# Kernel tuning notes

Measured on AMD Instinct MI355X. Metric: run time of the kernel, lower is better.

The kernel has to match this reference:

```python
import jax, jax.numpy as jnp
import numpy as np

N_NODES = 100000
N_EDGES = 1600000
IN_DIM = 128
HIDDEN = 128
N_CLASSES = 10
N_GRAPHS = 64


def _inv_sqrt_deg(deg):
    # DGL norm='both': 1/sqrt(deg), with inf (deg==0) clamped to 0
    return jnp.where(deg > 0, jax.lax.rsqrt(jnp.maximum(deg, 1.0)), 0.0)


def graph_conv(h, src, dst, W, b):
    # DGL GraphConv, norm='both': rst = D_in^{-1/2} A D_out^{-1/2} h W + b
    ones = jnp.ones((src.shape[0],), dtype=h.dtype)
    deg_out = jax.ops.segment_sum(ones, src, num_segments=N_NODES)
    deg_in = jax.ops.segment_sum(ones, dst, num_segments=N_NODES)
    h = h * _inv_sqrt_deg(deg_out)[:, None]          # src-side norm
    msg = h[src]                                      # gather [E, D]
    agg = jax.ops.segment_sum(msg, dst, num_segments=N_NODES)  # scatter-add
    agg = agg * _inv_sqrt_deg(deg_in)[:, None]        # dst-side norm
    return agg @ W + b


def avg_pool(h, graph_ids):
    sums = jax.ops.segment_sum(h, graph_ids, num_segments=N_GRAPHS)
    cnt = jax.ops.segment_sum(jnp.ones((h.shape[0],), h.dtype), graph_ids,
                              num_segments=N_GRAPHS)
    return sums / jnp.maximum(cnt, 1.0)[:, None]


def setup_inputs() -> dict:
    key = jax.random.key(0)
    ks = jax.random.split(key, 10)
    h = jax.random.normal(ks[0], (N_NODES, IN_DIM), dtype=jnp.float32)
    src = jax.random.randint(ks[1], (N_EDGES,), 0, N_NODES)
    dst = jax.random.randint(ks[2], (N_EDGES,), 0, N_NODES)
    graph_ids = jnp.sort(jax.random.randint(ks[3], (N_NODES,), 0, N_GRAPHS))
    s1 = 1.0 / np.sqrt(IN_DIM)
    s2 = 1.0 / np.sqrt(HIDDEN)
    W1 = jax.random.uniform(ks[4], (IN_DIM, HIDDEN), jnp.float32, -s1, s1)
    b1 = jnp.zeros((HIDDEN,), jnp.float32)
    W2 = jax.random.uniform(ks[5], (HIDDEN, HIDDEN), jnp.float32, -s2, s2)
    b2 = jnp.zeros((HIDDEN,), jnp.float32)
    Wc = jax.random.uniform(ks[6], (HIDDEN, N_CLASSES), jnp.float32, -s2, s2)
    bc = jnp.zeros((N_CLASSES,), jnp.float32)
    return {"h": h, "src": src, "dst": dst, "graph_ids": graph_ids,
            "W1": W1, "b1": b1, "W2": W2, "b2": b2, "Wc": Wc, "bc": bc}


def reference(h, src, dst, graph_ids, W1, b1, W2, b2, Wc, bc):
    h = jax.nn.relu(graph_conv(h, src, dst, W1, b1))
    h = jax.nn.relu(graph_conv(h, src, dst, W2, b2))
    hg = avg_pool(h, graph_ids)          # [N_GRAPHS, HIDDEN]
    return hg @ Wc + bc                  # [N_GRAPHS, N_CLASSES]
```

## Files before the change

kernel.cpp:

```cpp
#include <hip/hip_runtime.h>

#define N_NODES 100000
#define N_EDGES 1600000
#define DIM     128
#define NGRAPH  64
#define NCLS    10
#define ZROW    N_NODES

#define NBLK    64
#define EPB     (N_EDGES / NBLK)
#define RANGE   50000

typedef __bf16 bf16x8 __attribute__((ext_vector_type(8)));
typedef float  f32x4  __attribute__((ext_vector_type(4)));

__device__ __forceinline__ ushort f2bf(float x) {
  uint b = __float_as_uint(x);
  b += 0x7fffu + ((b >> 16) & 1u);
  return (ushort)(b >> 16);
}
__device__ __forceinline__ uint pack2(float lo, float hi) {
  return (uint)f2bf(lo) | ((uint)f2bf(hi) << 16);
}
__device__ __forceinline__ float unlo(uint u) { return __uint_as_float(u << 16); }
__device__ __forceinline__ float unhi(uint u) { return __uint_as_float(u & 0xffff0000u); }

__device__ __forceinline__ void acc8(float* a, uint4 u) {
  a[0] += unlo(u.x); a[1] += unhi(u.x);
  a[2] += unlo(u.y); a[3] += unhi(u.y);
  a[4] += unlo(u.z); a[5] += unhi(u.z);
  a[6] += unlo(u.w); a[7] += unhi(u.w);
}

__global__ void k_init(float* __restrict__ pool, float* __restrict__ cnt,
                       uint* __restrict__ padrow) {
  int t = threadIdx.x;
  for (int i = t; i < NGRAPH * DIM; i += 256) pool[i] = 0.f;
  if (t < NGRAPH) cnt[t] = 0.f;
  if (t < DIM / 2) padrow[t] = 0u;
}

__global__ __launch_bounds__(256)
void k_hist(const int* __restrict__ src, const int* __restrict__ dst,
            ushort* __restrict__ part) {
  extern __shared__ uint cnt[];
  int p = blockIdx.y;
  int b = blockIdx.x;
  const int* ids = (p < 2) ? dst : src;
  int base = (p & 1) * RANGE;
  for (int i = threadIdx.x; i < RANGE / 2; i += 256) cnt[i] = 0;
  __syncthreads();
  int cb = b * EPB;
  for (int j = threadIdx.x; j < EPB; j += 256) {
    int v = ids[cb + j] - base;
    if ((unsigned)v < RANGE) atomicAdd(&cnt[v >> 1], 1u << ((v & 1) * 16));
  }
  __syncthreads();
  uint* out = (uint*)(part + ((size_t)p * NBLK + b) * RANGE);
  for (int i = threadIdx.x; i < RANGE / 2; i += 256) out[i] = cnt[i];
}

__global__ void k_degsum(const ushort* __restrict__ part, int* __restrict__ deg_in,
                         int* __restrict__ deg_out, ushort* __restrict__ pre) {
  int n = blockIdx.x * 256 + threadIdx.x;
  if (n >= N_NODES) return;
  int r = n / RANGE, i = n % RANGE;
  const ushort* pin  = part + ((size_t)r * NBLK) * RANGE + i;
  const ushort* pout = part + ((size_t)(2 + r) * NBLK) * RANGE + i;
  int sin = 0, sout = 0;
  for (int b = 0; b < NBLK; ++b) {
    pre[(size_t)b * N_NODES + n] = (ushort)sin;
    sin  += pin[(size_t)b * RANGE];
    sout += pout[(size_t)b * RANGE];
  }
  deg_in[n] = sin;
  deg_out[n] = sout;
}

__global__ void k_blocksum(const int* __restrict__ deg_in, int* __restrict__ bsum) {
  __shared__ int s[256];
  int i = blockIdx.x * 256 + threadIdx.x;
  s[threadIdx.x] = (i < N_NODES) ? deg_in[i] : 0;
  __syncthreads();
  for (int off = 128; off > 0; off >>= 1) {
    if (threadIdx.x < off) s[threadIdx.x] += s[threadIdx.x + off];
    __syncthreads();
  }
  if (threadIdx.x == 0) bsum[blockIdx.x] = s[0];
}

__global__ void k_scan_bsum(int* __restrict__ bsum, int nb) {
  __shared__ int s[512];
  int t = threadIdx.x;
  int v = (t < nb) ? bsum[t] : 0;
  s[t] = v;
  __syncthreads();
  for (int off = 1; off < 512; off <<= 1) {
    int x = (t >= off) ? s[t - off] : 0;
    __syncthreads();
    s[t] += x;
    __syncthreads();
  }
  if (t < nb) bsum[t] = s[t] - v;
}

__global__ void k_rowptr(const int* __restrict__ deg_in, const int* __restrict__ bsum,
                         int* __restrict__ row_ptr) {
  __shared__ int s[256];
  int t = threadIdx.x;
  int i = blockIdx.x * 256 + t;
  int v = (i < N_NODES) ? deg_in[i] : 0;
  s[t] = v;
  __syncthreads();
  for (int off = 1; off < 256; off <<= 1) {
    int x = (t >= off) ? s[t - off] : 0;
    __syncthreads();
    s[t] += x;
    __syncthreads();
  }
  if (i < N_NODES) row_ptr[i] = bsum[blockIdx.x] + s[t] - v;
  if (i == N_NODES - 1) row_ptr[N_NODES] = bsum[blockIdx.x] + s[t];
}

__global__ __launch_bounds__(256)
void k_fillrank(const int* __restrict__ src, const int* __restrict__ dst,
                const int* __restrict__ row_ptr, const ushort* __restrict__ pre,
                int* __restrict__ csr_src) {
  extern __shared__ uint rk[];
  int b = blockIdx.x;
  int base = blockIdx.y * RANGE;
  for (int i = threadIdx.x; i < RANGE / 2; i += 256) rk[i] = 0;
  __syncthreads();
  int cb = b * EPB;
  for (int j = threadIdx.x; j < EPB; j += 256) {
    int d = dst[cb + j];
    int s = src[cb + j];
    int v = d - base;
    if ((unsigned)v < RANGE) {
      uint old = atomicAdd(&rk[v >> 1], 1u << ((v & 1) * 16));
      int rank = (old >> ((v & 1) * 16)) & 0xffff;
      int pos = row_ptr[d] + pre[(size_t)b * N_NODES + d] + rank;
      csr_src[pos] = s;
    }
  }
}

__global__ void k_convW(const float* __restrict__ W1, const float* __restrict__ W2,
                        ushort* __restrict__ Wt1, ushort* __restrict__ Wt2) {
  int idx = blockIdx.x * 256 + threadIdx.x;
  const float* W = (idx < 16384) ? W1 : W2;
  ushort* Wt = (idx < 16384) ? Wt1 : Wt2;
  int t = idx & 16383;
  int c = t >> 7, k = t & 127;
  Wt[c * 128 + k] = f2bf(W[k * 128 + c]);
}

__global__ void k_prescale(const float4* __restrict__ h4, const int* __restrict__ deg_out,
                           uint4* __restrict__ out4) {
  int idx = blockIdx.x * blockDim.x + threadIdx.x;
  if (idx < N_NODES * 16) {
    int row = idx >> 4;
    int d = deg_out[row];
    float s = d > 0 ? rsqrtf((float)d) : 0.f;
    float4 v0 = h4[idx * 2];
    float4 v1 = h4[idx * 2 + 1];
    uint4 o;
    o.x = pack2(v0.x * s, v0.y * s);
    o.y = pack2(v0.z * s, v0.w * s);
    o.z = pack2(v1.x * s, v1.y * s);
    o.w = pack2(v1.z * s, v1.w * s);
    out4[idx] = o;
  }
}

__global__ __launch_bounds__(256)
void k_gg(const uint* __restrict__ hs, const int* __restrict__ row_ptr,
          const int* __restrict__ csr_src, const ushort* __restrict__ Wt,
          const float* __restrict__ bias, const int* __restrict__ deg_scale,
          ushort* __restrict__ out) {
  __shared__ ushort As[16][136];
  int wv = threadIdx.x >> 6, lane = threadIdx.x & 63;
  int strip = blockIdx.x;
  int sub = lane >> 4, li = lane & 15;

  int lr = lane & 15, lk = lane >> 4;
  bf16x8 bfrag[4][2];
  #pragma unroll
  for (int ks = 0; ks < 4; ++ks)
    #pragma unroll
    for (int c2 = 0; c2 < 2; ++c2)
      bfrag[ks][c2] = *(const bf16x8*)(Wt + (size_t)((wv * 2 + c2) * 16 + lr) * 128 +
                                       ks * 32 + lk * 8);

  #pragma unroll
  for (int it = 0; it < 4; ++it) {
    int n = strip * 16 + wv * 4 + it;
    int beg = row_ptr[n], end = row_ptr[n + 1], deg = end - beg;
    float a[8] = {};
    for (int cb2 = 0; cb2 < deg; cb2 += 64) {
      int cdeg = min(64, deg - cb2);
      int myidx = (lane < cdeg) ? csr_src[beg + cb2 + lane] : ZROW;
      for (int e = 0; e < cdeg; e += 16) {
        int s0 = __shfl(myidx, e + sub);
        int s1 = __shfl(myidx, e + 4 + sub);
        int s2 = __shfl(myidx, e + 8 + sub);
        int s3 = __shfl(myidx, e + 12 + sub);
        uint4 u0 = *(const uint4*)(hs + (size_t)s0 * 64 + li * 4);
        uint4 u1 = *(const uint4*)(hs + (size_t)s1 * 64 + li * 4);
        uint4 u2 = *(const uint4*)(hs + (size_t)s2 * 64 + li * 4);
        uint4 u3 = *(const uint4*)(hs + (size_t)s3 * 64 + li * 4);
        acc8(a, u0); acc8(a, u1); acc8(a, u2); acc8(a, u3);
      }
    }
    #pragma unroll
    for (int k = 0; k < 8; ++k) {
      a[k] += __shfl_xor(a[k], 16);
      a[k] += __shfl_xor(a[k], 32);
    }
    if (sub == 0) {
      float sc = deg > 0 ? rsqrtf((float)deg) : 0.f;
      uint4 o;
      o.x = pack2(a[0] * sc, a[1] * sc);
      o.y = pack2(a[2] * sc, a[3] * sc);
      o.z = pack2(a[4] * sc, a[5] * sc);
      o.w = pack2(a[6] * sc, a[7] * sc);
      *(uint4*)&As[wv * 4 + it][li * 8] = o;
    }
  }
  __syncthreads();

  f32x4 acc[2] = {};
  #pragma unroll
  for (int ks = 0; ks < 4; ++ks) {
    bf16x8 af = *(const bf16x8*)&As[lr][ks * 32 + lk * 8];
    acc[0] = __builtin_amdgcn_mfma_f32_16x16x32_bf16(af, bfrag[ks][0], acc[0], 0, 0, 0);
    acc[1] = __builtin_amdgcn_mfma_f32_16x16x32_bf16(af, bfrag[ks][1], acc[1], 0, 0, 0);
  }

  #pragma unroll
  for (int rr = 0; rr < 4; ++rr) {
    int row = strip * 16 + lk * 4 + rr;
    float s = 1.f;
    if (deg_scale) {
      int d = deg_scale[row];
      s = d > 0 ? rsqrtf((float)d) : 0.f;
    }
    #pragma unroll
    for (int c2 = 0; c2 < 2; ++c2) {
      int col = (wv * 2 + c2) * 16 + lr;
      float v = fmaxf(acc[c2][rr] + bias[col], 0.f) * s;
      out[(size_t)row * 128 + col] = f2bf(v);
    }
  }
}

__global__ __launch_bounds__(256)
void k_pool(const uint* __restrict__ h, const int* __restrict__ gid,
            float* __restrict__ pool, float* __restrict__ cnt) {
  int wave = threadIdx.x >> 6, lane = threadIdx.x & 63;
  int start = blockIdx.x * 256 + wave * 64;
  if (start >= N_NODES) return;
  int end = min(start + 64, N_NODES);
  float ax = 0.f, ay = 0.f;
  int g = gid[start];
  int seglen = 0;
  for (int i = start; i < end; ++i) {
    int gi = gid[i];
    if (gi != g) {
      atomicAdd(&pool[g * DIM + 2 * lane], ax);
      atomicAdd(&pool[g * DIM + 2 * lane + 1], ay);
      if (lane == 0) atomicAdd(&cnt[g], (float)seglen);
      ax = ay = 0.f;
      seglen = 0;
      g = gi;
    }
    uint u = h[(size_t)i * 64 + lane];
    ax += unlo(u);
    ay += unhi(u);
    ++seglen;
  }
  atomicAdd(&pool[g * DIM + 2 * lane], ax);
  atomicAdd(&pool[g * DIM + 2 * lane + 1], ay);
  if (lane == 0) atomicAdd(&cnt[g], (float)seglen);
}

__global__ void k_classifier(const float* __restrict__ pool, const float* __restrict__ cnt,
                             const float* __restrict__ Wc, const float* __restrict__ bc,
                             float* __restrict__ out) {
  int t = threadIdx.x;
  if (t >= NGRAPH * NCLS) return;
  int g = t / NCLS, c = t % NCLS;
  float inv = 1.f / fmaxf(cnt[g], 1.f);
  float s = bc[c];
  for (int k = 0; k < DIM; ++k) s += pool[g * DIM + k] * inv * Wc[k * NCLS + c];
  out[g * NCLS + c] = s;
}

extern "C" void kernel_launch(void* const* d_in, const int* in_sizes, int n_in,
                              void* d_out, int out_size, void* d_ws, size_t ws_size,
                              hipStream_t stream) {
  const float* h   = (const float*)d_in[0];
  const int* src   = (const int*)d_in[1];
  const int* dst   = (const int*)d_in[2];
  const int* gid   = (const int*)d_in[3];
  const float* W1  = (const float*)d_in[4];
  const float* b1  = (const float*)d_in[5];
  const float* W2  = (const float*)d_in[6];
  const float* b2  = (const float*)d_in[7];
  const float* Wc  = (const float*)d_in[8];
  const float* bc  = (const float*)d_in[9];
  float* out = (float*)d_out;

  size_t off = 0;
  auto alloc = [&](size_t bytes) -> char* {
    char* p = (char*)d_ws + off;
    off += (bytes + 255) & ~(size_t)255;
    return p;
  };
  ushort* h2buf   = (ushort*)alloc((size_t)N_NODES * DIM * 2);
  int*    csr_src = (int*)alloc((size_t)N_EDGES * 4);
  int*    row_ptr = (int*)alloc((size_t)(N_NODES + 1) * 4);
  int*    bsum    = (int*)alloc(512 * 4);
  ushort* Wt1     = (ushort*)alloc(16384 * 2);
  ushort* Wt2     = (ushort*)alloc(16384 * 2);
  ushort* hbuf    = (ushort*)alloc((size_t)(N_NODES + 1) * DIM * 2);
  uint*   padrow  = (uint*)(hbuf + (size_t)N_NODES * DIM);
  ushort* part    = (ushort*)alloc((size_t)4 * NBLK * RANGE * 2);
  ushort* h1buf   = part;
  ushort* pre     = (ushort*)alloc((size_t)NBLK * N_NODES * 2);
  int*    deg_out = (int*)alloc((size_t)N_NODES * 4);
  int*    deg_in  = (int*)alloc((size_t)N_NODES * 4);
  float*  pool    = (float*)alloc((size_t)NGRAPH * DIM * 4);
  float*  cnt     = (float*)alloc((size_t)NGRAPH * 4);
  (void)ws_size; (void)in_sizes; (void)n_in; (void)out_size;

  const int NB = (N_NODES + 255) / 256;
  const size_t HIST_LDS = (RANGE / 2) * sizeof(uint);

  k_init<<<1, 256, 0, stream>>>(pool, cnt, padrow);
  k_hist<<<dim3(NBLK, 4), 256, HIST_LDS, stream>>>(src, dst, part);
  k_degsum<<<NB, 256, 0, stream>>>(part, deg_in, deg_out, pre);
  k_blocksum<<<NB, 256, 0, stream>>>(deg_in, bsum);
  k_scan_bsum<<<1, 512, 0, stream>>>(bsum, NB);
  k_rowptr<<<NB, 256, 0, stream>>>(deg_in, bsum, row_ptr);
  k_fillrank<<<dim3(NBLK, 2), 256, HIST_LDS, stream>>>(src, dst, row_ptr, pre, csr_src);
  k_convW<<<128, 256, 0, stream>>>(W1, W2, Wt1, Wt2);
  k_prescale<<<(N_NODES * 16 + 255) / 256, 256, 0, stream>>>((const float4*)h, deg_out,
                                                             (uint4*)hbuf);
  k_gg<<<N_NODES / 16, 256, 0, stream>>>((const uint*)hbuf, row_ptr, csr_src,
                                         Wt1, b1, deg_out, h1buf);
  k_gg<<<N_NODES / 16, 256, 0, stream>>>((const uint*)h1buf, row_ptr, csr_src,
                                         Wt2, b2, nullptr, h2buf);
  k_pool<<<(N_NODES + 255) / 256, 256, 0, stream>>>((const uint*)h2buf, gid, pool, cnt);
  k_classifier<<<1, 640, 0, stream>>>(pool, cnt, Wc, bc, out);
}
```

Baseline: 433.2 us.

## Assign one node per 16-lane group in fused gather-GEMM, prefetch next index chunk

The gather phase previously processed four nodes sequentially per wave, with all 64 lanes splitting each node's edges and reducing via cross-lane shuffles. Now each 16-lane quarter-wave handles its own node concurrently over 16-edge chunks, so the xor-shuffle reduction goes away. The next chunk of CSR source indices is prefetched while the current chunk is processed. This exposes more independent gathers in flight per wave, at the cost of load imbalance between quarter-waves when node degrees differ.

```diff
diff --git a/kernel.cpp b/kernel.cpp
--- a/kernel.cpp
+++ b/kernel.cpp
@@ -181,7 +181,44 @@
   __shared__ ushort As[16][136];
   int wv = threadIdx.x >> 6, lane = threadIdx.x & 63;
   int strip = blockIdx.x;
-  int sub = lane >> 4, li = lane & 15;
+  int g = lane >> 4;
+  int li = lane & 15;
+  int glane = g * 16;
+
+  int n = strip * 16 + wv * 4 + g;
+  int beg = row_ptr[n];
+  int deg = row_ptr[n + 1] - beg;
+
+  float a[8] = {};
+
+  int nxt = (li < deg) ? csr_src[beg + li] : ZROW;
+  for (int cb = 0; cb < deg; cb += 16) {
+    int idx = nxt;
+    int rem = deg - cb - 16;
+    if (rem > 0) nxt = (li < rem) ? csr_src[beg + cb + 16 + li] : ZROW;
+    #pragma unroll
+    for (int e = 0; e < 16; e += 4) {
+      int s0 = __shfl(idx, glane + e);
+      int s1 = __shfl(idx, glane + e + 1);
+      int s2 = __shfl(idx, glane + e + 2);
+      int s3 = __shfl(idx, glane + e + 3);
+      uint4 u0 = *(const uint4*)(hs + (size_t)s0 * 64 + li * 4);
+      uint4 u1 = *(const uint4*)(hs + (size_t)s1 * 64 + li * 4);
+      uint4 u2 = *(const uint4*)(hs + (size_t)s2 * 64 + li * 4);
+      uint4 u3 = *(const uint4*)(hs + (size_t)s3 * 64 + li * 4);
+      acc8(a, u0); acc8(a, u1); acc8(a, u2); acc8(a, u3);
+    }
+  }
+
+  {
+    float sc = deg > 0 ? rsqrtf((float)deg) : 0.f;
+    uint4 o;
+    o.x = pack2(a[0] * sc, a[1] * sc);
+    o.y = pack2(a[2] * sc, a[3] * sc);
+    o.z = pack2(a[4] * sc, a[5] * sc);
+    o.w = pack2(a[6] * sc, a[7] * sc);
+    *(uint4*)&As[wv * 4 + g][li * 8] = o;
+  }
 
   int lr = lane & 15, lk = lane >> 4;
   bf16x8 bfrag[4][2];
@@ -191,42 +228,6 @@
     for (int c2 = 0; c2 < 2; ++c2)
       bfrag[ks][c2] = *(const bf16x8*)(Wt + (size_t)((wv * 2 + c2) * 16 + lr) * 128 +
                                        ks * 32 + lk * 8);
-
-  #pragma unroll
-  for (int it = 0; it < 4; ++it) {
-    int n = strip * 16 + wv * 4 + it;
-    int beg = row_ptr[n], end = row_ptr[n + 1], deg = end - beg;
-    float a[8] = {};
-    for (int cb2 = 0; cb2 < deg; cb2 += 64) {
-      int cdeg = min(64, deg - cb2);
-      int myidx = (lane < cdeg) ? csr_src[beg + cb2 + lane] : ZROW;
-      for (int e = 0; e < cdeg; e += 16) {
-        int s0 = __shfl(myidx, e + sub);
-        int s1 = __shfl(myidx, e + 4 + sub);
-        int s2 = __shfl(myidx, e + 8 + sub);
-        int s3 = __shfl(myidx, e + 12 + sub);
-        uint4 u0 = *(const uint4*)(hs + (size_t)s0 * 64 + li * 4);
-        uint4 u1 = *(const uint4*)(hs + (size_t)s1 * 64 + li * 4);
-        uint4 u2 = *(const uint4*)(hs + (size_t)s2 * 64 + li * 4);
-        uint4 u3 = *(const uint4*)(hs + (size_t)s3 * 64 + li * 4);
-        acc8(a, u0); acc8(a, u1); acc8(a, u2); acc8(a, u3);
-      }
-    }
-    #pragma unroll
-    for (int k = 0; k < 8; ++k) {
-      a[k] += __shfl_xor(a[k], 16);
-      a[k] += __shfl_xor(a[k], 32);
-    }
-    if (sub == 0) {
-      float sc = deg > 0 ? rsqrtf((float)deg) : 0.f;
-      uint4 o;
-      o.x = pack2(a[0] * sc, a[1] * sc);
-      o.y = pack2(a[2] * sc, a[3] * sc);
-      o.z = pack2(a[4] * sc, a[5] * sc);
-      o.w = pack2(a[6] * sc, a[7] * sc);
-      *(uint4*)&As[wv * 4 + it][li * 8] = o;
-    }
-  }
   __syncthreads();
 
   f32x4 acc[2] = {};
```

New measurement: 435.3 us. No clear change (+0.5%).
